# Optimization experiments

Hardware: AMD Instinct MI355X
Metric: run time of the kernel (lower is better)

## Reference

```python
import jax, jax.numpy as jnp
import numpy as np

H = 16
D_MODEL = 1024
D_K = D_MODEL // H


def setup_inputs() -> dict:
    key = jax.random.key(0)
    kx, kq, kk, kv, ko = jax.random.split(key, 5)
    B, T = 4, 2048
    scale = 1.0 / np.sqrt(D_MODEL)
    return {
        "X": jax.random.normal(kx, (B, T, D_MODEL), dtype=jnp.float32),
        "W_q": jax.random.normal(kq, (D_MODEL, D_MODEL), dtype=jnp.float32) * scale,
        "W_k": jax.random.normal(kk, (D_MODEL, D_MODEL), dtype=jnp.float32) * scale,
        "W_v": jax.random.normal(kv, (D_MODEL, D_MODEL), dtype=jnp.float32) * scale,
        "W_o": jax.random.normal(ko, (D_MODEL, D_MODEL), dtype=jnp.float32) * scale,
    }


def reference(X, W_q, W_k, W_v, W_o):
    B, T, D = X.shape
    # projections (torch Linear: x @ W.T); weights stored as [out, in]=[D,D]
    Q = (X @ W_q.T).reshape(B, T, H, D_K).transpose(0, 2, 1, 3)  # [B,H,T,Dk]
    K = (X @ W_k.T).reshape(B, T, H, D_K).transpose(0, 2, 1, 3)
    V = (X @ W_v.T).reshape(B, T, H, D_K).transpose(0, 2, 1, 3)
    S = jnp.einsum("bhqd,bhkd->bhqk", Q, K) * (D_K ** -0.5)  # [B,H,T,T]
    causal = jnp.tril(jnp.ones((T, T), dtype=bool))
    S = jnp.where(causal, S, -jnp.inf)
    A = jax.nn.softmax(S, axis=-1)
    out = jnp.einsum("bhqk,bhkd->bhqd", A, V)  # [B,H,T,Dk]
    out = out.transpose(0, 2, 1, 3).reshape(B, T, D)
    return out @ W_o.T
```

## Files before the change

### kernel.cpp

```cpp
#include <hip/hip_runtime.h>
#include <hip/hip_bf16.h>

#define T_SEQ 2048
#define NB 4
#define NH 16
#define DK 64
#define DM 1024
#define QKS 2048

typedef __attribute__((ext_vector_type(8))) __bf16 bf16x8;
typedef __attribute__((ext_vector_type(4))) __bf16 bf16x4;
typedef __attribute__((ext_vector_type(4))) float f32x4;
typedef __attribute__((ext_vector_type(2))) int i32x2;
typedef __attribute__((ext_vector_type(4))) int i32x4;

__device__ __forceinline__ void gl_lds16(const __bf16* g, __bf16* l) {
  __builtin_amdgcn_global_load_lds(
      (const __attribute__((address_space(1))) void*)g,
      (__attribute__((address_space(3))) void*)l,
      16, 0, 0);
}

__device__ __forceinline__ unsigned cvt_pk_bf16(float lo, float hi) {
  unsigned r;
  asm("v_cvt_pk_bf16_f32 %0, %1, %2" : "=v"(r) : "v"(lo), "v"(hi));
  return r;
}

__global__ __launch_bounds__(256) void cast_f32_to_bf16(const float* __restrict__ in,
                                                        __bf16* __restrict__ out, int n4) {
  int i = blockIdx.x * 256 + threadIdx.x;
  if (i >= n4) return;
  float4 v = reinterpret_cast<const float4*>(in)[i];
  bf16x4 o;
  o[0] = (__bf16)v.x; o[1] = (__bf16)v.y; o[2] = (__bf16)v.z; o[3] = (__bf16)v.w;
  reinterpret_cast<bf16x4*>(out)[i] = o;
}

__global__ __launch_bounds__(256) void cast_weights(const float* __restrict__ a,
                                                    const float* __restrict__ b,
                                                    const float* __restrict__ c,
                                                    const float* __restrict__ d,
                                                    __bf16* __restrict__ oa,
                                                    __bf16* __restrict__ ob,
                                                    __bf16* __restrict__ oc,
                                                    __bf16* __restrict__ od) {
  const int which = blockIdx.y;
  const float* in = (which == 0) ? a : (which == 1) ? b : (which == 2) ? c : d;
  __bf16* out = (which == 0) ? oa : (which == 1) ? ob : (which == 2) ? oc : od;
  int i = blockIdx.x * 256 + threadIdx.x;
  float4 v = reinterpret_cast<const float4*>(in)[i];
  bf16x4 o;
  o[0] = (__bf16)v.x; o[1] = (__bf16)v.y; o[2] = (__bf16)v.z; o[3] = (__bf16)v.w;
  reinterpret_cast<bf16x4*>(out)[i] = o;
}

template<int DO_QSCALE>
__global__ __launch_bounds__(512, 2) void gemm_nt_8p(const __bf16* __restrict__ A,
                                                     const __bf16* __restrict__ Bm,
                                                     __bf16* __restrict__ C,
                                                     int M, int N, int K) {
  __shared__ alignas(16) __bf16 As[2][256][64];
  __shared__ alignas(16) __bf16 Bs[2][256][64];
  const int tid = threadIdx.x;
  const int wid = tid >> 6, l = tid & 63, lg = l >> 4, lr = l & 15;
  const int wm = wid >> 2, wn = wid & 3;
  const int f = (int)blockIdx.x;
  const int cpx = (int)gridDim.x >> 3;
  const int swz = (f & 7) * cpx + (f >> 3);
  const int nbn = N >> 8;
  const int m0 = (swz / nbn) << 8, n0 = (swz % nbn) << 8;

  const int srow = l >> 3;
  const int schunk = (l & 7) ^ srow;
  const int rsw = lr & 7;
  const int strow = wid * 8 + srow;

  f32x4 acc[8][4] = {};
  bf16x8 aA[8], bB[8];

  auto SA = [&](int buf, int half, int t) {
    #pragma unroll
    for (int j = 0; j < 2; ++j)
      gl_lds16(A + (size_t)(m0 + half * 128 + j * 64 + strow) * K + t * 64 + schunk * 8,
               &As[buf][half * 128 + j * 64 + wid * 8][0]);
  };
  auto SB = [&](int buf, int half, int t) {
    #pragma unroll
    for (int j = 0; j < 2; ++j)
      gl_lds16(Bm + (size_t)(n0 + half * 128 + j * 64 + strow) * K + t * 64 + schunk * 8,
               &Bs[buf][half * 128 + j * 64 + wid * 8][0]);
  };
  auto LA = [&](int buf, int mh) {
    #pragma unroll
    for (int mt = 0; mt < 4; ++mt) {
      const char* p = (const char*)&As[buf][wm * 128 + mh * 64 + mt * 16 + lr][0];
      aA[mt * 2 + 0] = *reinterpret_cast<const bf16x8*>(p + ((lg ^ rsw) << 4));
      aA[mt * 2 + 1] = *reinterpret_cast<const bf16x8*>(p + (((4 + lg) ^ rsw) << 4));
    }
  };
  auto LB = [&](int buf) {
    #pragma unroll
    for (int nt = 0; nt < 4; ++nt) {
      const char* p = (const char*)&Bs[buf][wn * 64 + nt * 16 + lr][0];
      bB[nt * 2 + 0] = *reinterpret_cast<const bf16x8*>(p + ((lg ^ rsw) << 4));
      bB[nt * 2 + 1] = *reinterpret_cast<const bf16x8*>(p + (((4 + lg) ^ rsw) << 4));
    }
  };
  auto MQ = [&](int mh, int nh) {
    #pragma unroll
    for (int mt = 0; mt < 4; ++mt)
      #pragma unroll
      for (int ntl = 0; ntl < 2; ++ntl) {
        const int nt = nh * 2 + ntl;
        acc[mh * 4 + mt][nt] = __builtin_amdgcn_mfma_f32_16x16x32_bf16(
            aA[mt * 2 + 0], bB[nt * 2 + 0], acc[mh * 4 + mt][nt], 0, 0, 0);
        acc[mh * 4 + mt][nt] = __builtin_amdgcn_mfma_f32_16x16x32_bf16(
            aA[mt * 2 + 1], bB[nt * 2 + 1], acc[mh * 4 + mt][nt], 0, 0, 0);
      }
  };

  SB(0, 0, 0); SB(0, 1, 0); SA(0, 0, 0); SA(0, 1, 0);
  SB(1, 0, 1); SB(1, 1, 1); SA(1, 0, 1);
  asm volatile("s_waitcnt vmcnt(6)" ::: "memory");
  __builtin_amdgcn_s_barrier();

  const int NIT = K >> 7;
  for (int i = 0; i < NIT; ++i) {
    const bool lastit = (i == NIT - 1);
    const int t2 = 2 * i + 2, t3 = 2 * i + 3;
    LA(0, 0); LB(0);
    SA(1, 1, 2 * i + 1);
    __builtin_amdgcn_s_barrier();
    asm volatile("s_waitcnt lgkmcnt(0)" ::: "memory");
    __builtin_amdgcn_sched_barrier(0);
    __builtin_amdgcn_s_setprio(1); MQ(0, 0); __builtin_amdgcn_s_setprio(0);
    __builtin_amdgcn_s_barrier();
    if (!lastit) SB(0, 0, t2);
    __builtin_amdgcn_s_setprio(1); MQ(0, 1); __builtin_amdgcn_s_setprio(0);
    __builtin_amdgcn_s_barrier();
    LA(0, 1);
    if (!lastit) SB(0, 1, t2);
    __builtin_amdgcn_s_barrier();
    asm volatile("s_waitcnt lgkmcnt(0)" ::: "memory");
    __builtin_amdgcn_sched_barrier(0);
    __builtin_amdgcn_s_setprio(1); MQ(1, 1); __builtin_amdgcn_s_setprio(0);
    __builtin_amdgcn_s_barrier();
    if (!lastit) SA(0, 0, t2);
    __builtin_amdgcn_s_setprio(1); MQ(1, 0); __builtin_amdgcn_s_setprio(0);
    if (lastit) asm volatile("s_waitcnt vmcnt(0)" ::: "memory");
    else        asm volatile("s_waitcnt vmcnt(6)" ::: "memory");
    __builtin_amdgcn_s_barrier();
    LA(1, 0); LB(1);
    if (!lastit) SA(0, 1, t2);
    __builtin_amdgcn_s_barrier();
    asm volatile("s_waitcnt lgkmcnt(0)" ::: "memory");
    __builtin_amdgcn_sched_barrier(0);
    __builtin_amdgcn_s_setprio(1); MQ(0, 0); __builtin_amdgcn_s_setprio(0);
    __builtin_amdgcn_s_barrier();
    if (!lastit) SB(1, 0, t3);
    __builtin_amdgcn_s_setprio(1); MQ(0, 1); __builtin_amdgcn_s_setprio(0);
    __builtin_amdgcn_s_barrier();
    LA(1, 1);
    if (!lastit) SB(1, 1, t3);
    __builtin_amdgcn_s_barrier();
    asm volatile("s_waitcnt lgkmcnt(0)" ::: "memory");
    __builtin_amdgcn_sched_barrier(0);
    __builtin_amdgcn_s_setprio(1); MQ(1, 1); __builtin_amdgcn_s_setprio(0);
    __builtin_amdgcn_s_barrier();
    if (!lastit) SA(1, 0, t3);
    __builtin_amdgcn_s_setprio(1); MQ(1, 0); __builtin_amdgcn_s_setprio(0);
    if (!lastit) asm volatile("s_waitcnt vmcnt(6)" ::: "memory");
    __builtin_amdgcn_s_barrier();
  }

  #pragma unroll
  for (int mt = 0; mt < 8; ++mt)
    #pragma unroll
    for (int nt = 0; nt < 4; ++nt) {
      const int ng = n0 + wn * 64 + nt * 16 + lr;
      const float sc = (DO_QSCALE && ng < 1024) ? 0.18033688f : 1.0f;
      #pragma unroll
      for (int r = 0; r < 4; ++r) {
        const int mg = m0 + wm * 128 + mt * 16 + 4 * lg + r;
        C[(size_t)mg * N + ng] = (__bf16)(acc[mt][nt][r] * sc);
      }
    }
}

template<typename CT, int MODE>
__global__ __launch_bounds__(256, 2) void gemm_nt(const __bf16* __restrict__ A,
                                                  const __bf16* __restrict__ B,
                                                  CT* __restrict__ C,
                                                  int M, int N, int K) {
  __shared__ alignas(16) __bf16 As[128][64];
  __shared__ alignas(16) __bf16 Bs[128][64];
  const int tid = threadIdx.x;
  const int m0 = blockIdx.y * 128, n0 = blockIdx.x * 128;
  const int w = tid >> 6, l = tid & 63, lg = l >> 4, lr = l & 15;
  const int wr = (w >> 1) * 64, wc = (w & 1) * 64;
  const int srow = l >> 3;
  const int schunk = (l & 7) ^ srow;

  f32x4 acc[4][4] = {};
  const int rsw = lr & 7;

  for (int k0 = 0; k0 < K; k0 += 64) {
    __syncthreads();
    #pragma unroll
    for (int j = 0; j < 4; ++j) {
      const int rbase = (w * 4 + j) * 8;
      gl_lds16(A + (size_t)(m0 + rbase + srow) * K + k0 + schunk * 8, &As[rbase][0]);
      gl_lds16(B + (size_t)(n0 + rbase + srow) * K + k0 + schunk * 8, &Bs[rbase][0]);
    }
    asm volatile("s_waitcnt vmcnt(0)" ::: "memory");
    __syncthreads();
    #pragma unroll
    for (int kk = 0; kk < 2; ++kk) {
      bf16x8 af[4], bfr[4];
      #pragma unroll
      for (int mt = 0; mt < 4; ++mt) {
        const char* p = (const char*)&As[wr + mt * 16 + lr][0];
        af[mt] = *reinterpret_cast<const bf16x8*>(p + (((kk * 4 + lg) ^ rsw) << 4));
      }
      #pragma unroll
      for (int nt = 0; nt < 4; ++nt) {
        const char* p = (const char*)&Bs[wc + nt * 16 + lr][0];
        bfr[nt] = *reinterpret_cast<const bf16x8*>(p + (((kk * 4 + lg) ^ rsw) << 4));
      }
      __builtin_amdgcn_s_setprio(1);
      #pragma unroll
      for (int mt = 0; mt < 4; ++mt)
        #pragma unroll
        for (int nt = 0; nt < 4; ++nt)
          acc[mt][nt] = __builtin_amdgcn_mfma_f32_16x16x32_bf16(af[mt], bfr[nt], acc[mt][nt], 0, 0, 0);
      __builtin_amdgcn_s_setprio(0);
    }
  }
  #pragma unroll
  for (int mt = 0; mt < 4; ++mt)
    #pragma unroll
    for (int nt = 0; nt < 4; ++nt)
      #pragma unroll
      for (int r = 0; r < 4; ++r) {
        const int mg = m0 + wr + mt * 16 + 4 * lg + r;
        int ng = n0 + wc + nt * 16 + lr;
        if (MODE == 2)
          ng = (ng & ~31) | (8 * (lr >> 2) + (lr & 3) + ((nt & 1) << 2));
        C[(size_t)mg * N + ng] = (CT)acc[mt][nt][r];
      }
}

__global__ __launch_bounds__(256, 2) void attn_fwd(const __bf16* __restrict__ QK,
                                                   const __bf16* __restrict__ VT,
                                                   __bf16* __restrict__ AO) {
  __shared__ alignas(16) __bf16 Ks[2][64][64];
  __shared__ alignas(16) __bf16 Vs[2][64][64];
  const int tid = threadIdx.x;
  const int w = tid >> 6, l = tid & 63, lg = l >> 4, lr = l & 15;

  const int fl = (int)blockIdx.x + 8 * (int)blockIdx.y;
  const int bh = ((fl & 7) << 3) | ((fl >> 3) & 7);
  const int c = fl >> 6;
  const int b = bh >> 4, h = bh & 15;
  const size_t bT = (size_t)b * T_SEQ;
  const int M = NB * T_SEQ;

  const int srow = l >> 3;
  const int schunk = (l & 7) ^ srow;
  const __bf16* Kg = QK + bT * QKS + 1024 + h * DK;
  const __bf16* Vg = VT + (size_t)(h * DK) * M + bT;
  const int rsw = lr & 7;

  bf16x8 vone;
  #pragma unroll
  for (int j = 0; j < 8; ++j) vone[j] = (__bf16)1.0f;

  const int qbA = c, qbB = 15 - c, qbC = 16 + c, qbD = 31 - c;
  const int qrwA = qbA * 64 + w * 16, qrwB = qbB * 64 + w * 16;
  const int qrwC = qbC * 64 + w * 16, qrwD = qbD * 64 + w * 16;
  const int klA = qbA * 64, klB = qbB * 64, klC = qbC * 64, klD = qbD * 64;

  const __bf16* QpA = QK + (bT + qrwA + lr) * QKS + h * DK;
  const __bf16* QpB = QK + (bT + qrwB + lr) * QKS + h * DK;
  const __bf16* QpC = QK + (bT + qrwC + lr) * QKS + h * DK;
  const __bf16* QpD = QK + (bT + qrwD + lr) * QKS + h * DK;
  const bf16x8 qfA0 = *reinterpret_cast<const bf16x8*>(QpA + 8 * lg);
  const bf16x8 qfA1 = *reinterpret_cast<const bf16x8*>(QpA + 32 + 8 * lg);
  const bf16x8 qfB0 = *reinterpret_cast<const bf16x8*>(QpB + 8 * lg);
  const bf16x8 qfB1 = *reinterpret_cast<const bf16x8*>(QpB + 32 + 8 * lg);
  const bf16x8 qfC0 = *reinterpret_cast<const bf16x8*>(QpC + 8 * lg);
  const bf16x8 qfC1 = *reinterpret_cast<const bf16x8*>(QpC + 32 + 8 * lg);
  const bf16x8 qfD0 = *reinterpret_cast<const bf16x8*>(QpD + 8 * lg);
  const bf16x8 qfD1 = *reinterpret_cast<const bf16x8*>(QpD + 32 + 8 * lg);

  f32x4 o_accA[4] = {}, o_accB[4] = {}, o_accC[4] = {}, o_accD[4] = {};
  f32x4 lA = {}, lB = {}, lC = {}, lD = {};

  auto STAGE = [&](int buf, int kbase) {
    #pragma unroll
    for (int i = 0; i < 2; ++i) {
      const int seg = w * 2 + i;
      gl_lds16(Kg + (size_t)(kbase + seg * 8 + srow) * QKS + schunk * 8,
               &Ks[buf][seg * 8][0]);
      gl_lds16(Vg + (size_t)(seg * 8 + srow) * M + kbase + schunk * 8,
               &Vs[buf][seg * 8][0]);
    }
  };

  auto CHUNK = [&](const bf16x8& qf0, const bf16x8& qf1, f32x4* o_acc,
                   f32x4& l_acc, int qrw, bool masked, int k0,
                   const bf16x8* kf, const bf16x8* vf) {
    f32x4 s[4] = {};
    __builtin_amdgcn_s_setprio(1);
    #pragma unroll
    for (int ct = 0; ct < 4; ++ct) {
      s[ct] = __builtin_amdgcn_mfma_f32_16x16x32_bf16(kf[2 * ct], qf0, s[ct], 0, 0, 0);
      s[ct] = __builtin_amdgcn_mfma_f32_16x16x32_bf16(kf[2 * ct + 1], qf1, s[ct], 0, 0, 0);
    }
    __builtin_amdgcn_s_setprio(0);
    if (masked) {
      #pragma unroll
      for (int ct = 0; ct < 4; ++ct)
        #pragma unroll
        for (int r = 0; r < 4; ++r)
          if (k0 + 16 * ct + 4 * lg + r > qrw + lr) s[ct][r] = -1e30f;
    }
    unsigned pk[4][2];
    #pragma unroll
    for (int ct = 0; ct < 4; ++ct) {
      const float p0 = __builtin_amdgcn_exp2f(s[ct][0]);
      const float p1 = __builtin_amdgcn_exp2f(s[ct][1]);
      const float p2 = __builtin_amdgcn_exp2f(s[ct][2]);
      const float p3 = __builtin_amdgcn_exp2f(s[ct][3]);
      pk[ct][0] = cvt_pk_bf16(p0, p1);
      pk[ct][1] = cvt_pk_bf16(p2, p3);
    }
    const bf16x8 pf0 = __builtin_bit_cast(bf16x8, i32x4{(int)pk[0][0], (int)pk[0][1],
                                                        (int)pk[1][0], (int)pk[1][1]});
    const bf16x8 pf1 = __builtin_bit_cast(bf16x8, i32x4{(int)pk[2][0], (int)pk[2][1],
                                                        (int)pk[3][0], (int)pk[3][1]});
    __builtin_amdgcn_s_setprio(1);
    l_acc = __builtin_amdgcn_mfma_f32_16x16x32_bf16(pf0, vone, l_acc, 0, 0, 0);
    l_acc = __builtin_amdgcn_mfma_f32_16x16x32_bf16(pf1, vone, l_acc, 0, 0, 0);
    #pragma unroll
    for (int dt = 0; dt < 4; ++dt) {
      o_acc[dt] = __builtin_amdgcn_mfma_f32_16x16x32_bf16(pf0, vf[2 * dt],     o_acc[dt], 0, 0, 0);
      o_acc[dt] = __builtin_amdgcn_mfma_f32_16x16x32_bf16(pf1, vf[2 * dt + 1], o_acc[dt], 0, 0, 0);
    }
    __builtin_amdgcn_s_setprio(0);
  };

  STAGE(0, 0);
  asm volatile("s_waitcnt vmcnt(0)" ::: "memory");
  __syncthreads();
  int buf = 0;

  for (int k0 = 0; k0 <= klD; k0 += 64) {
    if (k0 + 64 <= klD) STAGE(buf ^ 1, k0 + 64);

    bf16x8 kf[8], vf[8];
    #pragma unroll
    for (int ct = 0; ct < 4; ++ct) {
      const char* kb = (const char*)&Ks[buf][ct * 16 + lr][0];
      kf[2 * ct]     = *reinterpret_cast<const bf16x8*>(kb + ((lg ^ rsw) << 4));
      kf[2 * ct + 1] = *reinterpret_cast<const bf16x8*>(kb + (((lg + 4) ^ rsw) << 4));
      const char* vb = (const char*)&Vs[buf][ct * 16 + lr][0];
      vf[2 * ct]     = *reinterpret_cast<const bf16x8*>(vb + ((lg ^ rsw) << 4));
      vf[2 * ct + 1] = *reinterpret_cast<const bf16x8*>(vb + (((lg + 4) ^ rsw) << 4));
    }

    CHUNK(qfD0, qfD1, o_accD, lD, qrwD, k0 == klD, k0, kf, vf);
    if (k0 <= klC) CHUNK(qfC0, qfC1, o_accC, lC, qrwC, k0 == klC, k0, kf, vf);
    if (k0 <= klB) CHUNK(qfB0, qfB1, o_accB, lB, qrwB, k0 == klB, k0, kf, vf);
    if (k0 <= klA) CHUNK(qfA0, qfA1, o_accA, lA, qrwA, k0 == klA, k0, kf, vf);

    asm volatile("s_waitcnt vmcnt(0)" ::: "memory");
    __syncthreads();
    buf ^= 1;
  }

  #pragma unroll
  for (int cc = 0; cc < 4; ++cc) {
    const f32x4& la = (cc == 0) ? lA : (cc == 1) ? lB : (cc == 2) ? lC : lD;
    f32x4* oa = (cc == 0) ? o_accA : (cc == 1) ? o_accB : (cc == 2) ? o_accC : o_accD;
    const int qrw = (cc == 0) ? qrwA : (cc == 1) ? qrwB : (cc == 2) ? qrwC : qrwD;
    #pragma unroll
    for (int r = 0; r < 4; ++r) {
      const float inv = 1.0f / la[r];
      #pragma unroll
      for (int dt = 0; dt < 4; ++dt) {
        const int rg = qrw + 4 * lg + r;
        const int cg = h * DK + dt * 16 + lr;
        AO[(bT + rg) * DM + cg] = (__bf16)(oa[dt][r] * inv);
      }
    }
  }
}

extern "C" void kernel_launch(void* const* d_in, const int* in_sizes, int n_in,
                              void* d_out, int out_size, void* d_ws, size_t ws_size,
                              hipStream_t stream) {
  (void)in_sizes; (void)n_in; (void)out_size; (void)ws_size;
  const float* X  = (const float*)d_in[0];
  const float* Wq = (const float*)d_in[1];
  const float* Wk = (const float*)d_in[2];
  const float* Wv = (const float*)d_in[3];
  const float* Wo = (const float*)d_in[4];
  float* OUT = (float*)d_out;

  char* ws = (char*)d_ws;
  const size_t SZ_X  = (size_t)NB * T_SEQ * DM * 2;
  const size_t SZ_W  = (size_t)DM * DM * 2;
  const size_t SZ_QK = (size_t)NB * T_SEQ * QKS * 2;
  __bf16* Xb  = (__bf16*)ws; ws += SZ_X;
  __bf16* Wqb = (__bf16*)ws; ws += SZ_W;
  __bf16* Wkb = (__bf16*)ws; ws += SZ_W;
  __bf16* Wvb = (__bf16*)ws; ws += SZ_W;
  __bf16* Wob = (__bf16*)ws; ws += SZ_W;
  __bf16* QKb = (__bf16*)ws; ws += SZ_QK;
  __bf16* VTb = (__bf16*)ws; ws += SZ_X;
  __bf16* AOb = (__bf16*)ws; ws += SZ_X;

  const int M = NB * T_SEQ;

  cast_f32_to_bf16<<<(M * DM / 4) / 256, 256, 0, stream>>>(X, Xb, M * DM / 4);
  cast_weights<<<dim3(DM * DM / 4 / 256, 4), 256, 0, stream>>>(Wq, Wk, Wv, Wo,
                                                               Wqb, Wkb, Wvb, Wob);

  gemm_nt_8p<1><<<(M / 256) * (QKS / 256), 512, 0, stream>>>(Xb, Wqb, QKb, M, QKS, DM);
  gemm_nt<__bf16, 2><<<dim3(M / 128, DM / 128), 256, 0, stream>>>(Wvb, Xb, VTb, DM, M, DM);
  attn_fwd<<<dim3(8, NB * NH), 256, 0, stream>>>(QKb, VTb, AOb);
  gemm_nt<float, 0><<<dim3(DM / 128, M / 128), 256, 0, stream>>>(AOb, Wob, OUT, M, DM, DM);
}
```

Measured before the change: 143.2 us.

## Merge cast kernels and split B-fragment LDS reads in QK GEMM pipeline

Folds the separate X and weight f32-to-bf16 cast launches into one combined kernel, removing a launch. In the 8-phase QK projection GEMM, B fragments are now read from LDS in two halves, right before each MFMA half that uses them. Both global-to-LDS loads for the next B tile are issued together after the second half is read, so the buffer is not overwritten while still being read. This rebalances the LDS read and global load schedule across the phases, at the cost of an extra lgkmcnt wait in each half-iteration.

```diff
diff --git a/kernel.cpp b/kernel.cpp
--- a/kernel.cpp
+++ b/kernel.cpp
@@ -27,32 +27,35 @@
   return r;
 }
 
-__global__ __launch_bounds__(256) void cast_f32_to_bf16(const float* __restrict__ in,
-                                                        __bf16* __restrict__ out, int n4) {
+__global__ __launch_bounds__(256) void cast_all(const float* __restrict__ X,
+                                                const float* __restrict__ Wq,
+                                                const float* __restrict__ Wk,
+                                                const float* __restrict__ Wv,
+                                                const float* __restrict__ Wo,
+                                                __bf16* __restrict__ Xb,
+                                                __bf16* __restrict__ Wqb,
+                                                __bf16* __restrict__ Wkb,
+                                                __bf16* __restrict__ Wvb,
+                                                __bf16* __restrict__ Wob) {
+  const int NX4 = NB * T_SEQ * DM / 4;
+  const int NW4 = DM * DM / 4;
   int i = blockIdx.x * 256 + threadIdx.x;
-  if (i >= n4) return;
-  float4 v = reinterpret_cast<const float4*>(in)[i];
+  const float* in;
+  __bf16* out;
+  int idx;
+  if (i < NX4) {
+    in = X; out = Xb; idx = i;
+  } else {
+    const int j = i - NX4;
+    const int w = j >> 18;
+    idx = j & (NW4 - 1);
+    in = (w == 0) ? Wq : (w == 1) ? Wk : (w == 2) ? Wv : Wo;
+    out = (w == 0) ? Wqb : (w == 1) ? Wkb : (w == 2) ? Wvb : Wob;
+  }
+  float4 v = reinterpret_cast<const float4*>(in)[idx];
   bf16x4 o;
   o[0] = (__bf16)v.x; o[1] = (__bf16)v.y; o[2] = (__bf16)v.z; o[3] = (__bf16)v.w;
-  reinterpret_cast<bf16x4*>(out)[i] = o;
-}
-
-__global__ __launch_bounds__(256) void cast_weights(const float* __restrict__ a,
-                                                    const float* __restrict__ b,
-                                                    const float* __restrict__ c,
-                                                    const float* __restrict__ d,
-                                                    __bf16* __restrict__ oa,
-                                                    __bf16* __restrict__ ob,
-                                                    __bf16* __restrict__ oc,
-                                                    __bf16* __restrict__ od) {
-  const int which = blockIdx.y;
-  const float* in = (which == 0) ? a : (which == 1) ? b : (which == 2) ? c : d;
-  __bf16* out = (which == 0) ? oa : (which == 1) ? ob : (which == 2) ? oc : od;
-  int i = blockIdx.x * 256 + threadIdx.x;
-  float4 v = reinterpret_cast<const float4*>(in)[i];
-  bf16x4 o;
-  o[0] = (__bf16)v.x; o[1] = (__bf16)v.y; o[2] = (__bf16)v.z; o[3] = (__bf16)v.w;
-  reinterpret_cast<bf16x4*>(out)[i] = o;
+  reinterpret_cast<bf16x4*>(out)[idx] = o;
 }
 
 template<int DO_QSCALE>
@@ -99,9 +102,10 @@
       aA[mt * 2 + 1] = *reinterpret_cast<const bf16x8*>(p + (((4 + lg) ^ rsw) << 4));
     }
   };
-  auto LB = [&](int buf) {
-    #pragma unroll
-    for (int nt = 0; nt < 4; ++nt) {
+  auto LBh = [&](int buf, int nh) {
+    #pragma unroll
+    for (int ntl = 0; ntl < 2; ++ntl) {
+      const int nt = nh * 2 + ntl;
       const char* p = (const char*)&Bs[buf][wn * 64 + nt * 16 + lr][0];
       bB[nt * 2 + 0] = *reinterpret_cast<const bf16x8*>(p + ((lg ^ rsw) << 4));
       bB[nt * 2 + 1] = *reinterpret_cast<const bf16x8*>(p + (((4 + lg) ^ rsw) << 4));
@@ -119,6 +123,8 @@
             aA[mt * 2 + 1], bB[nt * 2 + 1], acc[mh * 4 + mt][nt], 0, 0, 0);
       }
   };
+  #define WAIT_LGKM() do { asm volatile("s_waitcnt lgkmcnt(0)" ::: "memory"); \
+                           __builtin_amdgcn_sched_barrier(0); } while (0)
 
   SB(0, 0, 0); SB(0, 1, 0); SA(0, 0, 0); SA(0, 1, 0);
   SB(1, 0, 1); SB(1, 1, 1); SA(1, 0, 1);
@@ -129,21 +135,20 @@
   for (int i = 0; i < NIT; ++i) {
     const bool lastit = (i == NIT - 1);
     const int t2 = 2 * i + 2, t3 = 2 * i + 3;
-    LA(0, 0); LB(0);
+    LA(0, 0); LBh(0, 0);
     SA(1, 1, 2 * i + 1);
     __builtin_amdgcn_s_barrier();
-    asm volatile("s_waitcnt lgkmcnt(0)" ::: "memory");
-    __builtin_amdgcn_sched_barrier(0);
+    WAIT_LGKM();
     __builtin_amdgcn_s_setprio(1); MQ(0, 0); __builtin_amdgcn_s_setprio(0);
     __builtin_amdgcn_s_barrier();
-    if (!lastit) SB(0, 0, t2);
+    LBh(0, 1);
+    WAIT_LGKM();
     __builtin_amdgcn_s_setprio(1); MQ(0, 1); __builtin_amdgcn_s_setprio(0);
     __builtin_amdgcn_s_barrier();
     LA(0, 1);
-    if (!lastit) SB(0, 1, t2);
-    __builtin_amdgcn_s_barrier();
-    asm volatile("s_waitcnt lgkmcnt(0)" ::: "memory");
-    __builtin_amdgcn_sched_barrier(0);
+    if (!lastit) { SB(0, 0, t2); SB(0, 1, t2); }
+    __builtin_amdgcn_s_barrier();
+    WAIT_LGKM();
     __builtin_amdgcn_s_setprio(1); MQ(1, 1); __builtin_amdgcn_s_setprio(0);
     __builtin_amdgcn_s_barrier();
     if (!lastit) SA(0, 0, t2);
@@ -151,21 +156,20 @@
     if (lastit) asm volatile("s_waitcnt vmcnt(0)" ::: "memory");
     else        asm volatile("s_waitcnt vmcnt(6)" ::: "memory");
     __builtin_amdgcn_s_barrier();
-    LA(1, 0); LB(1);
+    LA(1, 0); LBh(1, 0);
     if (!lastit) SA(0, 1, t2);
     __builtin_amdgcn_s_barrier();
-    asm volatile("s_waitcnt lgkmcnt(0)" ::: "memory");
-    __builtin_amdgcn_sched_barrier(0);
+    WAIT_LGKM();
     __builtin_amdgcn_s_setprio(1); MQ(0, 0); __builtin_amdgcn_s_setprio(0);
     __builtin_amdgcn_s_barrier();
-    if (!lastit) SB(1, 0, t3);
+    LBh(1, 1);
+    WAIT_LGKM();
     __builtin_amdgcn_s_setprio(1); MQ(0, 1); __builtin_amdgcn_s_setprio(0);
     __builtin_amdgcn_s_barrier();
     LA(1, 1);
-    if (!lastit) SB(1, 1, t3);
-    __builtin_amdgcn_s_barrier();
-    asm volatile("s_waitcnt lgkmcnt(0)" ::: "memory");
-    __builtin_amdgcn_sched_barrier(0);
+    if (!lastit) { SB(1, 0, t3); SB(1, 1, t3); }
+    __builtin_amdgcn_s_barrier();
+    WAIT_LGKM();
     __builtin_amdgcn_s_setprio(1); MQ(1, 1); __builtin_amdgcn_s_setprio(0);
     __builtin_amdgcn_s_barrier();
     if (!lastit) SA(1, 0, t3);
@@ -186,6 +190,7 @@
         C[(size_t)mg * N + ng] = (__bf16)(acc[mt][nt][r] * sc);
       }
     }
+  #undef WAIT_LGKM
 }
 
 template<typename CT, int MODE>
@@ -424,9 +429,8 @@
 
   const int M = NB * T_SEQ;
 
-  cast_f32_to_bf16<<<(M * DM / 4) / 256, 256, 0, stream>>>(X, Xb, M * DM / 4);
-  cast_weights<<<dim3(DM * DM / 4 / 256, 4), 256, 0, stream>>>(Wq, Wk, Wv, Wo,
-                                                               Wqb, Wkb, Wvb, Wob);
+  cast_all<<<(M * DM / 4 + 4 * DM * DM / 4) / 256, 256, 0, stream>>>(
+      X, Wq, Wk, Wv, Wo, Xb, Wqb, Wkb, Wvb, Wob);
 
   gemm_nt_8p<1><<<(M / 256) * (QKS / 256), 512, 0, stream>>>(Xb, Wqb, QKb, M, QKS, DM);
   gemm_nt<__bf16, 2><<<dim3(M / 128, DM / 128), 256, 0, stream>>>(Wvb, Xb, VTb, DM, M, DM);
```

New measurement: 143.3 us. No clear change (+0.1%).
